# Optimization experiments

Hardware: AMD Instinct MI355X
Metric: run time of the kernel (lower is better)

## Reference

```python
import jax, jax.numpy as jnp
import numpy as np

B, NORM_NC, LABEL_NC, H, W, SL = 8, 256, 19, 64, 64, 512
EPS = 1e-5


def _conv5(x, w, b):
    # 5x5 'same' conv, NCHW / OIHW
    y = jax.lax.conv_general_dilated(x, w, (1, 1), [(2, 2), (2, 2)],
                                     dimension_numbers=('NCHW', 'OIHW', 'NCHW'))
    return y + b[None, :, None, None]


def _instance_norm(x):
    # InstanceNorm2d(affine=False): per-sample, per-channel over HxW, biased var
    m = x.mean(axis=(2, 3), keepdims=True)
    v = x.var(axis=(2, 3), keepdims=True)
    return (x - m) / jnp.sqrt(v + EPS)


def setup_inputs() -> dict:
    key = jax.random.key(0)
    ks = jax.random.split(key, 12)
    # one-hot semantic segmentation map (what segmap.bool() assumes in practice)
    labels = jax.random.randint(ks[0], (B, H, W), 0, LABEL_NC)
    segmap = jax.nn.one_hot(labels, LABEL_NC, axis=1, dtype=jnp.float32)  # [B,19,H,W]
    s = 0.02
    return {
        'x': jax.random.normal(ks[1], (B, NORM_NC, H, W), jnp.float32),
        'segmap': segmap,
        'style_codes': jax.random.normal(ks[2], (B, LABEL_NC, SL), jnp.float32),
        'fc_w': jax.random.normal(ks[3], (LABEL_NC, SL, SL), jnp.float32) * s,
        'fc_b': jnp.zeros((LABEL_NC, SL), jnp.float32),
        'conv_gamma_w': jax.random.normal(ks[4], (NORM_NC, SL, 5, 5), jnp.float32) * s,
        'conv_gamma_b': jnp.zeros((NORM_NC,), jnp.float32),
        'conv_beta_w': jax.random.normal(ks[5], (NORM_NC, SL, 5, 5), jnp.float32) * s,
        'conv_beta_b': jnp.zeros((NORM_NC,), jnp.float32),
        'spade_shared_w': jax.random.normal(ks[6], (512, LABEL_NC, 5, 5), jnp.float32) * s,
        'spade_shared_b': jnp.zeros((512,), jnp.float32),
        'spade_gamma_w': jax.random.normal(ks[7], (NORM_NC, 512, 5, 5), jnp.float32) * s,
        'spade_gamma_b': jnp.zeros((NORM_NC,), jnp.float32),
        'spade_beta_w': jax.random.normal(ks[8], (NORM_NC, 512, 5, 5), jnp.float32) * s,
        'spade_beta_b': jnp.zeros((NORM_NC,), jnp.float32),
        'blending_gamma': jnp.zeros((1,), jnp.float32),
        'blending_beta': jnp.zeros((1,), jnp.float32),
    }


def reference(x, segmap, style_codes, fc_w, fc_b,
              conv_gamma_w, conv_gamma_b, conv_beta_w, conv_beta_b,
              spade_shared_w, spade_shared_b,
              spade_gamma_w, spade_gamma_b, spade_beta_w, spade_beta_b,
              blending_gamma, blending_beta):
    normalized = _instance_norm(x)
    # F.interpolate(segmap, size=x.shape[2:], mode='nearest') is identity here
    # (segmap already has x's spatial size).
    mask = segmap > 0  # segmap.bool(): [B,J,H,W]
    J = mask.shape[1]

    # per-class style MLP: mu[b,j] = relu(fc_mu_j(style_codes[b,j]))
    mu = jax.nn.relu(jnp.einsum('bjd,jed->bje', style_codes, fc_w) + fc_b)  # [B,J,SL]

    # for overlapping masks; pixels with no class stay zero.
    last_idx = (J - 1) - jnp.argmax(mask[:, ::-1], axis=1)  # [B,H,W] last true j
    any_m = mask.any(axis=1)                                 # [B,H,W]
    mu_sel = mu[jnp.arange(mu.shape[0])[:, None, None], last_idx]  # [B,H,W,SL]
    middle_avg = jnp.where(any_m[..., None], mu_sel, 0.0).transpose(0, 3, 1, 2)

    gamma_avg = _conv5(middle_avg, conv_gamma_w, conv_gamma_b)
    beta_avg = _conv5(middle_avg, conv_beta_w, conv_beta_b)

    actv = jax.nn.relu(_conv5(segmap, spade_shared_w, spade_shared_b))
    gamma_spade = _conv5(actv, spade_gamma_w, spade_gamma_b)
    beta_spade = _conv5(actv, spade_beta_w, spade_beta_b)

    ga = jax.nn.sigmoid(blending_gamma)  # shape (1,) broadcasts
    ba = jax.nn.sigmoid(blending_beta)
    gamma_final = ga * gamma_avg + (1 - ga) * gamma_spade
    beta_final = ba * beta_avg + (1 - ba) * beta_spade
    return normalized * (1 + gamma_final) + beta_final
```

## Files before the change

### kernel.cpp

```cpp
#include <hip/hip_runtime.h>
#include <hip/hip_bf16.h>
#include <stdint.h>

typedef __attribute__((__ext_vector_type__(8))) __bf16 bf16x8;
typedef __attribute__((__ext_vector_type__(2))) __bf16 bf16x2;
typedef __attribute__((__ext_vector_type__(4))) float  f32x4;
typedef __attribute__((__ext_vector_type__(8))) int    v8i;

#define SCALE_A_DW 0x77777777
#define SCALE_B_DW 0x79797979

__device__ __forceinline__ void gl_lds16(const void* g, void* l) {
  __builtin_amdgcn_global_load_lds(
      (__attribute__((address_space(1))) void*)(uintptr_t)g,
      (__attribute__((address_space(3))) void*)(unsigned)(uintptr_t)l,
      16, 0, 0);
}

__global__ __launch_bounds__(256) void k_prep(
    const float* __restrict__ x, float* __restrict__ stats,
    const float* __restrict__ seg, int* __restrict__ labels,
    const float* __restrict__ cgw, const float* __restrict__ cbw,
    float* __restrict__ wpa,
    const float* __restrict__ ssw, __bf16* __restrict__ wspb,
    __bf16* __restrict__ Aav) {
  __shared__ __align__(16) char smem[16*401*4];
  int blk = blockIdx.x;
  if (blk < 2048) {
    int bc = blk;
    const float4* p = (const float4*)(x + (size_t)bc * 4096);
    float s = 0.f, ss = 0.f;
    for (int i = threadIdx.x; i < 1024; i += 256) {
      float4 v = p[i];
      s  += v.x + v.y + v.z + v.w;
      ss += v.x*v.x + v.y*v.y + v.z*v.z + v.w*v.w;
    }
    #pragma unroll
    for (int o = 32; o > 0; o >>= 1) { s += __shfl_down(s, o); ss += __shfl_down(ss, o); }
    float* sh = (float*)smem;
    int wv = threadIdx.x >> 6;
    if ((threadIdx.x & 63) == 0) { sh[wv] = s; sh[4 + wv] = ss; }
    __syncthreads();
    if (threadIdx.x == 0) {
      float S = sh[0]+sh[1]+sh[2]+sh[3], SS = sh[4]+sh[5]+sh[6]+sh[7];
      float m = S * (1.f/4096.f);
      float var = SS * (1.f/4096.f) - m*m;
      stats[bc] = m;
      stats[2048 + bc] = rsqrtf(var + 1e-5f);
    }
  } else if (blk < 2176) {
    int idx = (blk - 2048)*256 + threadIdx.x;
    int b = idx >> 12, pix = idx & 4095;
    const float* p = seg + (size_t)b*19*4096 + pix;
    int lab = -1;
    for (int j = 0; j < 19; ++j) if (p[(size_t)j*4096] > 0.f) lab = j;
    labels[idx] = lab;
  } else if (blk < 3200) {
    int bid = blk - 2176;
    float* s = (float*)smem;
    int n0 = (bid & 31) * 16, c0 = (bid >> 5) * 16;
    for (int i = threadIdx.x; i < 6400; i += 256) {
      int nn = i / 400, qq = i % 400;
      int n = n0 + nn;
      const float* src = (n < 256) ? cgw + (size_t)n*12800 : cbw + (size_t)(n-256)*12800;
      s[nn*401 + qq] = src[c0*25 + qq];
    }
    __syncthreads();
    for (int i = threadIdx.x; i < 6400; i += 256) {
      int nn = i & 15, rest = i >> 4;
      int k5 = rest % 25, cc = rest / 25;
      wpa[((size_t)k5*512 + c0 + cc)*512 + n0 + nn] = s[nn*401 + cc*25 + k5];
    }
  } else if (blk < 4200) {
    int idx = (blk - 3200)*256 + threadIdx.x;
    int o = idx & 511, k5 = (idx >> 9) % 25, j = idx / 12800;
    wspb[idx] = (j < 19) ? (__bf16)ssw[((size_t)o*19 + j)*25 + k5] : (__bf16)0.f;
  } else {
    ((unsigned*)(Aav + 3800ull*512))[threadIdx.x] = 0;
  }
}

__global__ __launch_bounds__(512) void k_mu(const float* __restrict__ sc,
                                            const float* __restrict__ fcw,
                                            const float* __restrict__ fcb,
                                            float* __restrict__ mu) {
  int b = blockIdx.x / 19, j = blockIdx.x % 19;
  __shared__ float s[512];
  s[threadIdx.x] = sc[(b*19 + j)*512 + threadIdx.x];
  __syncthreads();
  int e = threadIdx.x;
  const float4* w4 = (const float4*)(fcw + ((size_t)(j*512 + e))*512);
  const float4* s4 = (const float4*)s;
  float acc = 0.f;
  for (int d = 0; d < 128; ++d) {
    float4 w = w4[d], v = s4[d];
    acc += w.x*v.x + w.y*v.y + w.z*v.z + w.w*v.w;
  }
  acc += fcb[j*512 + e];
  mu[(b*19 + j)*512 + e] = fmaxf(acc, 0.f);
}

__global__ __launch_bounds__(256) void k_pack_spade(
    const float* __restrict__ g, const float* __restrict__ bt,
    uint8_t* __restrict__ wq) {
  int n = blockIdx.x;
  const float* src = (n < 256) ? g + (size_t)n*12800 : bt + (size_t)(n-256)*12800;
  __shared__ float s[12800];
  for (int i = threadIdx.x; i < 12800; i += 256) s[i] = src[i];
  __syncthreads();
  int t = threadIdx.x;
  for (int k5 = 0; k5 < 25; ++k5) {
    float w0 = s[(2*t)*25 + k5] * 64.f, w1 = s[(2*t+1)*25 + k5] * 64.f;
    int pk = __builtin_amdgcn_cvt_pk_fp8_f32(w0, w1, 0, false);
    *(unsigned short*)(wq + ((size_t)k5*512 + n)*512 + 2*t) = (unsigned short)pk;
  }
}

__global__ __launch_bounds__(512) void k_A_avg(const float* __restrict__ mu,
                                               const float* __restrict__ wpa,
                                               __bf16* __restrict__ A) {
  int b = blockIdx.x / 25, k5 = blockIdx.x % 25;
  int n = threadIdx.x;
  const float* wp = wpa + (size_t)k5*262144 + n;
  const float* mub = mu + b*19*512;
  float acc[19];
  #pragma unroll
  for (int j = 0; j < 19; ++j) acc[j] = 0.f;
  for (int c = 0; c < 512; ++c) {
    float w = wp[(size_t)c*512];
    #pragma unroll
    for (int j = 0; j < 19; ++j) acc[j] += mub[j*512 + c] * w;
  }
  #pragma unroll
  for (int j = 0; j < 19; ++j)
    A[((size_t)((b*19 + j)*25 + k5))*512 + n] = (__bf16)acc[j];
}

__global__ void k_actv(const int* __restrict__ labels, const __bf16* __restrict__ wsp,
                       const float* __restrict__ ssb, uint8_t* __restrict__ actv) {
  int b = blockIdx.x / 68, hp = blockIdx.x % 68;
  int t = threadIdx.x;
  size_t rowbase = ((size_t)b*68 + hp)*68;
  if (hp < 2 || hp >= 66) {
    unsigned* dp = (unsigned*)(actv + rowbase*512);
    for (int i = t; i < 8704; i += 256) dp[i] = 0;
    return;
  }
  int h = hp - 2;
  __shared__ int lab[5*68];
  for (int i = t; i < 5*68; i += 256) {
    int dh = i / 68, xx = i % 68;
    int hh = h + dh - 2, ww = xx - 2;
    int l = 19;
    if (hh >= 0 && hh < 64 && ww >= 0 && ww < 64) {
      int l0 = labels[b*4096 + hh*64 + ww];
      if (l0 >= 0) l = l0;
    }
    lab[i] = l;
  }
  {
    unsigned* dp = (unsigned*)(actv + rowbase*512);
    dp[t] = 0; dp[66*128 + t] = 0;
  }
  __syncthreads();
  float bs0 = ssb[2*t], bs1 = ssb[2*t + 1];
  for (int w = 0; w < 64; ++w) {
    float a0 = bs0, a1 = bs1;
    #pragma unroll
    for (int tap = 0; tap < 25; ++tap) {
      int l = lab[(tap/5)*68 + w + (tap%5)];
      bf16x2 v = *(const bf16x2*)(wsp + (size_t)(l*25 + tap)*512 + 2*t);
      a0 += (float)v[0]; a1 += (float)v[1];
    }
    a0 = fmaxf(a0, 0.f) * 256.f;
    a1 = fmaxf(a1, 0.f) * 256.f;
    int pk = __builtin_amdgcn_cvt_pk_fp8_f32(a0, a1, 0, false);
    *(unsigned short*)(actv + (rowbase + 2 + w)*512 + 2*t) = (unsigned short)pk;
  }
}

__global__ __launch_bounds__(512) void k_conv(
    const uint8_t* __restrict__ actv, const uint8_t* __restrict__ wq,
    const float* __restrict__ sgb, const float* __restrict__ sbb,
    __bf16* __restrict__ gbs) {
  __shared__ __align__(16) uint8_t ldsA[2][32768];
  const int tid = threadIdx.x, wv = tid >> 6, lane = tid & 63;
  const int l15 = lane & 15, q = lane >> 4;
  const int m0 = blockIdx.x * 256, n0 = blockIdx.y * 256;
  const int b = m0 >> 12;

  int aoff[4], ldst[4];
  #pragma unroll
  for (int i = 0; i < 4; ++i) {
    int p = i*512 + tid;
    int r = p >> 3, pc = p & 7;
    int cl = pc ^ (r & 7);
    int pix = (m0 + r) & 4095;
    int h = pix >> 6, w = pix & 63;
    aoff[i] = ((b*68 + h)*68 + w)*512 + cl*16;
    ldst[i] = i*8192 + wv*1024;
  }

  const int wm = (wv >> 2) * 128, wn = (wv & 3) * 64;
  const uint8_t* wqb = wq + (size_t)(n0 + wn + l15)*512 + q*32;
  f32x4 acc[8][4] = {};

  auto stageA = [&](int t, int buf) {
    int k5 = t >> 2, kc = t & 3;
    int a_k = ((k5/5)*68 + (k5%5))*512 + kc*128;
    uint8_t* la = &ldsA[buf][0];
    #pragma unroll
    for (int i = 0; i < 4; ++i)
      gl_lds16(actv + aoff[i] + a_k, la + ldst[i]);
  };

  auto loadB = [&](int t, v8i* o) {
    const uint8_t* p = wqb + (t >> 2)*262144 + (t & 3)*128;
    #pragma unroll
    for (int ni = 0; ni < 4; ++ni)
      o[ni] = *(const v8i*)(p + ni*16*512);
  };

  auto compute = [&](int buf, const v8i* bfr) {
    __builtin_amdgcn_s_setprio(1);
    #pragma unroll
    for (int mi = 0; mi < 8; ++mi) {
      int row = wm + mi*16 + l15;
      const uint8_t* base = &ldsA[buf][row*128];
      union { v8i v; uint4 u[2]; } tt;
      tt.u[0] = *(const uint4*)(base + ((2*q    ) ^ (row & 7))*16);
      tt.u[1] = *(const uint4*)(base + ((2*q + 1) ^ (row & 7))*16);
      v8i af = tt.v;
      #pragma unroll
      for (int ni = 0; ni < 4; ++ni)
        acc[mi][ni] = __builtin_amdgcn_mfma_scale_f32_16x16x128_f8f6f4(
            af, bfr[ni], acc[mi][ni], 0, 0, 0, SCALE_A_DW, 0, SCALE_B_DW);
    }
    __builtin_amdgcn_s_setprio(0);
  };

  v8i bA[4], bB[4];
  stageA(0, 0); loadB(0, bA);
  stageA(1, 1); loadB(1, bB);
  #pragma unroll 1
  for (int t = 0; t < 98; t += 2) {
    asm volatile("s_waitcnt vmcnt(12)" ::: "memory");
    __builtin_amdgcn_s_barrier();
    __builtin_amdgcn_sched_barrier(0);
    compute(0, bA);
    __builtin_amdgcn_sched_barrier(0);
    __builtin_amdgcn_s_barrier();
    __builtin_amdgcn_sched_barrier(0);
    stageA(t + 2, 0); loadB(t + 2, bA);
    __builtin_amdgcn_sched_barrier(0);
    asm volatile("s_waitcnt vmcnt(12)" ::: "memory");
    __builtin_amdgcn_s_barrier();
    __builtin_amdgcn_sched_barrier(0);
    compute(1, bB);
    __builtin_amdgcn_sched_barrier(0);
    __builtin_amdgcn_s_barrier();
    __builtin_amdgcn_sched_barrier(0);
    stageA(t + 3, 1); loadB(t + 3, bB);
    __builtin_amdgcn_sched_barrier(0);
  }
  asm volatile("s_waitcnt vmcnt(12)" ::: "memory");
  __builtin_amdgcn_s_barrier();
  __builtin_amdgcn_sched_barrier(0);
  compute(0, bA);
  asm volatile("s_waitcnt vmcnt(0)" ::: "memory");
  __builtin_amdgcn_s_barrier();
  __builtin_amdgcn_sched_barrier(0);
  compute(1, bB);

  #pragma unroll
  for (int ni = 0; ni < 4; ++ni) {
    int n = n0 + wn + ni*16 + l15;
    float bias = (n < 256) ? sgb[n] : sbb[n - 256];
    #pragma unroll
    for (int mi = 0; mi < 8; ++mi) {
      int m = m0 + wm + mi*16 + q*4;
      size_t base = (size_t)m*512 + n;
      #pragma unroll
      for (int r = 0; r < 4; ++r)
        gbs[base + (size_t)r*512] = (__bf16)(acc[mi][ni][r] + bias);
    }
  }
}

__global__ __launch_bounds__(256) void k_gf(
    const int* __restrict__ labels, const __bf16* __restrict__ A,
    const float* __restrict__ cgb, const float* __restrict__ cbb,
    const __bf16* __restrict__ gbs, const float* __restrict__ x,
    const float* __restrict__ stats, const float* __restrict__ blg,
    const float* __restrict__ blb, float* __restrict__ out) {
  int wt = blockIdx.x & 3, h = (blockIdx.x >> 2) & 63, b = blockIdx.x >> 8;
  int w0 = wt * 16;
  __shared__ int rowbase[5*20];
  __shared__ __bf16 avg[16][512];
  __shared__ __bf16 spd[16][512];
  for (int i = threadIdx.x; i < 100; i += 256) {
    int dh = i / 20, xx = i % 20;
    int hh = h + dh - 2, ww = w0 + xx - 2;
    int l = (hh >= 0 && hh < 64 && ww >= 0 && ww < 64) ? labels[b*4096 + hh*64 + ww] : -1;
    rowbase[i] = (l >= 0) ? (b*19 + l)*25 : -1;
  }
  __syncthreads();
  int t = threadIdx.x;
  float bs0, bs1;
  if (2*t < 256) { bs0 = cgb[2*t]; bs1 = cgb[2*t + 1]; }
  else           { bs0 = cbb[2*t - 256]; bs1 = cbb[2*t - 255]; }
  size_t pixb = (size_t)b*4096 + h*64 + w0;
  for (int px = 0; px < 16; ++px) {
    float a0 = bs0, a1 = bs1;
    #pragma unroll
    for (int tap = 0; tap < 25; ++tap) {
      int rb = rowbase[(tap/5)*20 + px + (tap%5)];
      int row = (rb >= 0) ? rb + tap : 3800;
      bf16x2 v = *(const bf16x2*)(A + (size_t)row*512 + 2*t);
      a0 += (float)v[0]; a1 += (float)v[1];
    }
    avg[px][2*t]     = (__bf16)a0;
    avg[px][2*t + 1] = (__bf16)a1;
    *(bf16x2*)&spd[px][2*t] = *(const bf16x2*)(gbs + (pixb + px)*512 + 2*t);
  }
  __syncthreads();
  float ga = 1.f / (1.f + expf(-blg[0]));
  float ba = 1.f / (1.f + expf(-blb[0]));
  int c = threadIdx.x;
  int bc = b*256 + c;
  float mean = stats[bc], rstd = stats[2048 + bc];
  size_t xb = (size_t)bc*4096 + h*64 + w0;
  #pragma unroll
  for (int pq = 0; pq < 4; ++pq) {
    float4 xv = *(const float4*)(x + xb + pq*4);
    float4 ov;
    float* xo = (float*)&xv; float* oo = (float*)&ov;
    #pragma unroll
    for (int j = 0; j < 4; ++j) {
      int px = pq*4 + j;
      float gf  = ga*(float)avg[px][c]       + (1.f - ga)*(float)spd[px][c];
      float bf_ = ba*(float)avg[px][256 + c] + (1.f - ba)*(float)spd[px][256 + c];
      oo[j] = (xo[j] - mean)*rstd*(1.f + gf) + bf_;
    }
    *(float4*)(out + xb + pq*4) = ov;
  }
}

extern "C" void kernel_launch(void* const* d_in, const int* in_sizes, int n_in,
                              void* d_out, int out_size, void* d_ws, size_t ws_size,
                              hipStream_t stream) {
  const float* x    = (const float*)d_in[0];
  const float* seg  = (const float*)d_in[1];
  const float* sc   = (const float*)d_in[2];
  const float* fcw  = (const float*)d_in[3];
  const float* fcb  = (const float*)d_in[4];
  const float* cgw  = (const float*)d_in[5];
  const float* cgb  = (const float*)d_in[6];
  const float* cbw  = (const float*)d_in[7];
  const float* cbb  = (const float*)d_in[8];
  const float* ssw  = (const float*)d_in[9];
  const float* ssb  = (const float*)d_in[10];
  const float* sgw  = (const float*)d_in[11];
  const float* sgb  = (const float*)d_in[12];
  const float* sbw  = (const float*)d_in[13];
  const float* sbb  = (const float*)d_in[14];
  const float* blg  = (const float*)d_in[15];
  const float* blb  = (const float*)d_in[16];
  float* out = (float*)d_out;

  char* ws = (char*)d_ws;
  size_t off = 0;
  auto alloc = [&](size_t bytes) {
    void* p = ws + off; off += (bytes + 255) & ~(size_t)255; return p;
  };
  float*   stats = (float*)alloc(2048ull*2*4);
  int*     labels= (int*)  alloc(32768ull*4);
  float*   mu    = (float*)alloc(77824ull*4);
  __bf16*  Aav   = (__bf16*)alloc((3800ull + 1)*512*2);
  __bf16*  wspb  = (__bf16*)alloc(20ull*25*512*2);
  float*   wpa   = (float*)alloc(25ull*512*512*4);
  uint8_t* wq    = (uint8_t*)alloc(25ull*512*512);
  uint8_t* actv  = (uint8_t*)alloc(8ull*68*68*512);
  __bf16*  gbs   = (__bf16*)alloc(8ull*4096*512*2);

  k_prep      <<<4201, 256, 0, stream>>>(x, stats, seg, labels, cgw, cbw, wpa, ssw, wspb, Aav);
  k_mu        <<<152, 512, 0, stream>>>(sc, fcw, fcb, mu);
  k_pack_spade<<<512, 256, 0, stream>>>(sgw, sbw, wq);
  k_A_avg     <<<200, 512, 0, stream>>>(mu, wpa, Aav);
  k_actv      <<<544, 256, 0, stream>>>(labels, wspb, ssb, actv);
  k_conv      <<<dim3(128, 2), 512, 0, stream>>>(actv, wq, sgb, sbb, gbs);
  k_gf        <<<2048, 256, 0, stream>>>(labels, Aav, cgb, cbb, gbs, x, stats, blg, blb, out);
}
```

Before: 747.7 us.

## Restructure fp8 conv GEMM with 32x32 MFMA, LDS-staged B, ping-pong wave groups

The main fp8 implicit-GEMM conv kernel switches from 16x16x128 to 32x32x64 scaled MFMA and stages the weight (B) tiles through LDS with global_load_lds instead of direct per-lane global loads. It also uses a triple-buffered K pipeline of 64-byte chunks. The two wave groups are offset so that one reads LDS fragments while the other issues MFMAs, a ping-pong schedule. This aims to raise MFMA utilization and cut redundant global traffic for B. The cost is more barriers per iteration (200 iterations instead of 98 pairs) and a more fragile scheduling scheme.

```diff
diff --git a/kernel.cpp b/kernel.cpp
--- a/kernel.cpp
+++ b/kernel.cpp
@@ -5,6 +5,7 @@
 typedef __attribute__((__ext_vector_type__(8))) __bf16 bf16x8;
 typedef __attribute__((__ext_vector_type__(2))) __bf16 bf16x2;
 typedef __attribute__((__ext_vector_type__(4))) float  f32x4;
+typedef __attribute__((__ext_vector_type__(16))) float f32x16;
 typedef __attribute__((__ext_vector_type__(8))) int    v8i;
 
 #define SCALE_A_DW 0x77777777
@@ -183,106 +184,115 @@
     const uint8_t* __restrict__ actv, const uint8_t* __restrict__ wq,
     const float* __restrict__ sgb, const float* __restrict__ sbb,
     __bf16* __restrict__ gbs) {
-  __shared__ __align__(16) uint8_t ldsA[2][32768];
+  __shared__ __align__(16) uint8_t ldsA[3][16384];
+  __shared__ __align__(16) uint8_t ldsB[3][16384];
   const int tid = threadIdx.x, wv = tid >> 6, lane = tid & 63;
-  const int l15 = lane & 15, q = lane >> 4;
+  const int l31 = lane & 31, hh = lane >> 5;
   const int m0 = blockIdx.x * 256, n0 = blockIdx.y * 256;
   const int b = m0 >> 12;
-
-  int aoff[4], ldst[4];
+  const int g = wv >> 2;
+  const int wm = g * 128, wn = (wv & 3) * 64;
+
+  int aoff[2], boff[2], ldso[2];
   #pragma unroll
-  for (int i = 0; i < 4; ++i) {
+  for (int i = 0; i < 2; ++i) {
     int p = i*512 + tid;
-    int r = p >> 3, pc = p & 7;
-    int cl = pc ^ (r & 7);
+    int r = p >> 2, s = p & 3;
+    int c = s ^ (r & 3);
     int pix = (m0 + r) & 4095;
     int h = pix >> 6, w = pix & 63;
-    aoff[i] = ((b*68 + h)*68 + w)*512 + cl*16;
-    ldst[i] = i*8192 + wv*1024;
-  }
-
-  const int wm = (wv >> 2) * 128, wn = (wv & 3) * 64;
-  const uint8_t* wqb = wq + (size_t)(n0 + wn + l15)*512 + q*32;
-  f32x4 acc[8][4] = {};
-
-  auto stageA = [&](int t, int buf) {
-    int k5 = t >> 2, kc = t & 3;
-    int a_k = ((k5/5)*68 + (k5%5))*512 + kc*128;
-    uint8_t* la = &ldsA[buf][0];
-    #pragma unroll
-    for (int i = 0; i < 4; ++i)
-      gl_lds16(actv + aoff[i] + a_k, la + ldst[i]);
-  };
-
-  auto loadB = [&](int t, v8i* o) {
-    const uint8_t* p = wqb + (t >> 2)*262144 + (t & 3)*128;
-    #pragma unroll
-    for (int ni = 0; ni < 4; ++ni)
-      o[ni] = *(const v8i*)(p + ni*16*512);
-  };
-
-  auto compute = [&](int buf, const v8i* bfr) {
+    aoff[i] = ((b*68 + h)*68 + w)*512 + c*16;
+    boff[i] = (n0 + r)*512 + c*16;
+    ldso[i] = i*8192 + wv*1024;
+  }
+
+  f32x16 acc[4][2] = {};
+  v8i bfr[2], af01[2];
+
+  auto stage = [&](int t, int buf) {
+    int k5 = t >> 3, kc = t & 7;
+    int a_k = ((k5/5)*68 + (k5%5))*512 + kc*64;
+    int b_k = k5*262144 + kc*64;
+    #pragma unroll
+    for (int i = 0; i < 2; ++i) {
+      gl_lds16(actv + aoff[i] + a_k, &ldsA[buf][0] + ldso[i]);
+      gl_lds16(wq   + boff[i] + b_k, &ldsB[buf][0] + ldso[i]);
+    }
+  };
+
+  auto afrag = [&](int buf, int mi) -> v8i {
+    int r = wm + mi*32 + l31;
+    const uint8_t* base = &ldsA[buf][r*64];
+    union { v8i v; uint4 u[2]; } tt;
+    tt.u[0] = *(const uint4*)(base + ((2*hh    ) ^ (l31 & 3))*16);
+    tt.u[1] = *(const uint4*)(base + ((2*hh + 1) ^ (l31 & 3))*16);
+    return tt.v;
+  };
+  auto bfrag = [&](int buf, int ni) -> v8i {
+    int r = wn + ni*32 + l31;
+    const uint8_t* base = &ldsB[buf][r*64];
+    union { v8i v; uint4 u[2]; } tt;
+    tt.u[0] = *(const uint4*)(base + ((2*hh    ) ^ (l31 & 3))*16);
+    tt.u[1] = *(const uint4*)(base + ((2*hh + 1) ^ (l31 & 3))*16);
+    return tt.v;
+  };
+
+  auto readPhase = [&](int buf) {
+    bfr[0]  = bfrag(buf, 0); bfr[1]  = bfrag(buf, 1);
+    af01[0] = afrag(buf, 0); af01[1] = afrag(buf, 1);
+  };
+  auto mfmaPhase = [&](int buf) {
     __builtin_amdgcn_s_setprio(1);
     #pragma unroll
-    for (int mi = 0; mi < 8; ++mi) {
-      int row = wm + mi*16 + l15;
-      const uint8_t* base = &ldsA[buf][row*128];
-      union { v8i v; uint4 u[2]; } tt;
-      tt.u[0] = *(const uint4*)(base + ((2*q    ) ^ (row & 7))*16);
-      tt.u[1] = *(const uint4*)(base + ((2*q + 1) ^ (row & 7))*16);
-      v8i af = tt.v;
+    for (int mi = 0; mi < 2; ++mi)
       #pragma unroll
-      for (int ni = 0; ni < 4; ++ni)
-        acc[mi][ni] = __builtin_amdgcn_mfma_scale_f32_16x16x128_f8f6f4(
-            af, bfr[ni], acc[mi][ni], 0, 0, 0, SCALE_A_DW, 0, SCALE_B_DW);
-    }
+      for (int ni = 0; ni < 2; ++ni)
+        acc[mi][ni] = __builtin_amdgcn_mfma_scale_f32_32x32x64_f8f6f4(
+            af01[mi], bfr[ni], acc[mi][ni], 0, 0, 0, SCALE_A_DW, 0, SCALE_B_DW);
     __builtin_amdgcn_s_setprio(0);
-  };
-
-  v8i bA[4], bB[4];
-  stageA(0, 0); loadB(0, bA);
-  stageA(1, 1); loadB(1, bB);
+    v8i af2 = afrag(buf, 2), af3 = afrag(buf, 3);
+    __builtin_amdgcn_s_setprio(1);
+    #pragma unroll
+    for (int ni = 0; ni < 2; ++ni) {
+      acc[2][ni] = __builtin_amdgcn_mfma_scale_f32_32x32x64_f8f6f4(
+          af2, bfr[ni], acc[2][ni], 0, 0, 0, SCALE_A_DW, 0, SCALE_B_DW);
+      acc[3][ni] = __builtin_amdgcn_mfma_scale_f32_32x32x64_f8f6f4(
+          af3, bfr[ni], acc[3][ni], 0, 0, 0, SCALE_A_DW, 0, SCALE_B_DW);
+    }
+    __builtin_amdgcn_s_setprio(0);
+  };
+
+  stage(0, 0); stage(1, 1);
   #pragma unroll 1
-  for (int t = 0; t < 98; t += 2) {
-    asm volatile("s_waitcnt vmcnt(12)" ::: "memory");
+  for (int t = 0; t < 200; ++t) {
+    int buf = t % 3;
+    asm volatile("s_waitcnt vmcnt(4)" ::: "memory");
+    asm volatile("s_waitcnt lgkmcnt(0)" ::: "memory");
     __builtin_amdgcn_s_barrier();
-    __builtin_amdgcn_sched_barrier(0);
-    compute(0, bA);
-    __builtin_amdgcn_sched_barrier(0);
+    if (g == 0) readPhase(buf);
+    else if (t > 0) mfmaPhase((t + 2) % 3);
+    asm volatile("s_waitcnt lgkmcnt(0)" ::: "memory");
     __builtin_amdgcn_s_barrier();
-    __builtin_amdgcn_sched_barrier(0);
-    stageA(t + 2, 0); loadB(t + 2, bA);
-    __builtin_amdgcn_sched_barrier(0);
-    asm volatile("s_waitcnt vmcnt(12)" ::: "memory");
-    __builtin_amdgcn_s_barrier();
-    __builtin_amdgcn_sched_barrier(0);
-    compute(1, bB);
-    __builtin_amdgcn_sched_barrier(0);
-    __builtin_amdgcn_s_barrier();
-    __builtin_amdgcn_sched_barrier(0);
-    stageA(t + 3, 1); loadB(t + 3, bB);
-    __builtin_amdgcn_sched_barrier(0);
-  }
-  asm volatile("s_waitcnt vmcnt(12)" ::: "memory");
+    stage(t + 2 <= 199 ? t + 2 : 199, (t + 2) % 3);
+    if (g == 0) mfmaPhase(buf);
+    else readPhase(buf);
+  }
+  asm volatile("s_waitcnt lgkmcnt(0)" ::: "memory");
   __builtin_amdgcn_s_barrier();
-  __builtin_amdgcn_sched_barrier(0);
-  compute(0, bA);
-  asm volatile("s_waitcnt vmcnt(0)" ::: "memory");
-  __builtin_amdgcn_s_barrier();
-  __builtin_amdgcn_sched_barrier(0);
-  compute(1, bB);
+  if (g == 1) mfmaPhase(199 % 3);
 
   #pragma unroll
-  for (int ni = 0; ni < 4; ++ni) {
-    int n = n0 + wn + ni*16 + l15;
+  for (int ni = 0; ni < 2; ++ni) {
+    int n = n0 + wn + ni*32 + l31;
     float bias = (n < 256) ? sgb[n] : sbb[n - 256];
     #pragma unroll
-    for (int mi = 0; mi < 8; ++mi) {
-      int m = m0 + wm + mi*16 + q*4;
-      size_t base = (size_t)m*512 + n;
+    for (int mi = 0; mi < 4; ++mi) {
       #pragma unroll
-      for (int r = 0; r < 4; ++r)
-        gbs[base + (size_t)r*512] = (__bf16)(acc[mi][ni][r] + bias);
+      for (int j = 0; j < 16; ++j) {
+        int row = (j & 3) + 8*(j >> 2) + 4*hh;
+        int m = m0 + wm + mi*32 + row;
+        gbs[(size_t)m*512 + n] = (__bf16)(acc[mi][ni][j] + bias);
+      }
     }
   }
 }
```

Measured after the change: 694.2 us. 1.08x faster.
